# Optimization experiments

Measured on AMD Instinct MI355X. Metric: run time of the kernel, lower is better.

The kernel has to match this reference:

```python
import jax, jax.numpy as jnp
import numpy as np

EMBED_DIM = 384
NUM_HEADS = 6
EPS = 1e-5

def _conv_proj(x, w_dw, gamma, beta, mean, var, stride):
    # x: [B,H,W,C]; depthwise 3x3 conv (groups=C), pad 1, then BN (inference), then flatten HW.
    C = x.shape[-1]
    y = jax.lax.conv_general_dilated(
        x, w_dw, window_strides=(stride, stride), padding=[(1, 1), (1, 1)],
        dimension_numbers=("NHWC", "HWIO", "NHWC"), feature_group_count=C)
    y = (y - mean) * jax.lax.rsqrt(var + EPS) * gamma + beta
    B, H, W, Cc = y.shape
    return y.reshape(B, H * W, Cc)

def _heads(x):
    # [B, L, C] -> [B, nH, L, hd]
    B, L, C = x.shape
    hd = C // NUM_HEADS
    return x.reshape(B, L, NUM_HEADS, hd).transpose(0, 2, 1, 3)

def setup_inputs() -> dict:
    key = jax.random.key(0)
    ks = jax.random.split(key, 20)
    B, H, W, C = 64, 28, 28, EMBED_DIM
    inp = {
        "hidden_state": jax.random.normal(ks[0], (B, 1 + H * W, C), dtype=jnp.float32),
        "height": H,
        "width": W,
    }
    std = 0.02
    for i, p in enumerate(("q", "k", "v")):
        inp[f"w_dw_{p}"] = jax.random.normal(ks[1 + i], (3, 3, 1, C), dtype=jnp.float32) * std
        inp[f"bn_gamma_{p}"] = jnp.ones((C,), jnp.float32) + 0.1 * jax.random.normal(ks[4 + i], (C,))
        inp[f"bn_beta_{p}"] = 0.1 * jax.random.normal(ks[7 + i], (C,))
        inp[f"bn_mean_{p}"] = 0.1 * jax.random.normal(ks[10 + i], (C,))
        inp[f"bn_var_{p}"] = jnp.ones((C,), jnp.float32) + 0.1 * jax.random.uniform(ks[13 + i], (C,))
        inp[f"W_{p}"] = jax.random.normal(ks[16 + i], (C, C), dtype=jnp.float32) * std
        inp[f"b_{p}"] = jnp.zeros((C,), jnp.float32)
    return inp

def reference(hidden_state, height, width,
              w_dw_q, bn_gamma_q, bn_beta_q, bn_mean_q, bn_var_q, W_q, b_q,
              w_dw_k, bn_gamma_k, bn_beta_k, bn_mean_k, bn_var_k, W_k, b_k,
              w_dw_v, bn_gamma_v, bn_beta_v, bn_mean_v, bn_var_v, W_v, b_v):
    B, _, C = hidden_state.shape
    scale = C ** (-0.5)  # note: embed_dim**-0.5, as in the source
    cls_token = hidden_state[:, :1]
    x = hidden_state[:, 1:].reshape(B, height, width, C)

    q = _conv_proj(x, w_dw_q, bn_gamma_q, bn_beta_q, bn_mean_q, bn_var_q, stride=1)
    k = _conv_proj(x, w_dw_k, bn_gamma_k, bn_beta_k, bn_mean_k, bn_var_k, stride=2)
    v = _conv_proj(x, w_dw_v, bn_gamma_v, bn_beta_v, bn_mean_v, bn_var_v, stride=2)

    q = jnp.concatenate((cls_token, q), axis=1)
    k = jnp.concatenate((cls_token, k), axis=1)
    v = jnp.concatenate((cls_token, v), axis=1)

    q = _heads(q @ W_q + b_q)  # [B,h,Lq,d]
    k = _heads(k @ W_k + b_k)  # [B,h,Lk,d]
    v = _heads(v @ W_v + b_v)

    scores = jnp.einsum("bhqd,bhkd->bhqk", q, k) * scale
    probs = jax.nn.softmax(scores, axis=-1)
    ctx = jnp.einsum("bhqk,bhkd->bhqd", probs, v)
    Lq = ctx.shape[2]
    return ctx.transpose(0, 2, 1, 3).reshape(B, Lq, C)
```

## Files before the change

kernel.cpp:

```cpp
#include <hip/hip_runtime.h>
#include <hip/hip_bf16.h>

#define C_DIM 384
#define BATCH 64
#define LQ 785
#define LK 197
#define NHEADS 6
#define HDIM 64
#define QTILES 785
#define KTILES 197
#define KPAD 208

typedef __hip_bfloat16 bf16;
typedef __attribute__((ext_vector_type(8))) short short8;
typedef __attribute__((ext_vector_type(4))) float float4v;

__device__ __forceinline__ float bf2f(bf16 x) { return __bfloat162float(x); }
__device__ __forceinline__ bf16 f2bf(float x) { return __float2bfloat16(x); }
__device__ __forceinline__ float lo16f(unsigned int u) { return __uint_as_float(u << 16); }
__device__ __forceinline__ float hi16f(unsigned int u) { return __uint_as_float(u & 0xffff0000u); }
__device__ __forceinline__ unsigned short bfb(float x) {
    union { bf16 h; unsigned short s; } u; u.h = f2bf(x); return u.s;
}
__device__ __forceinline__ unsigned int pk2(float a, float b) {
    return ((unsigned int)bfb(b) << 16) | bfb(a);
}

template<bool F32>
__device__ __forceinline__ float ldx(const void* p, size_t i) {
    if constexpr (F32) return ((const float*)p)[i];
    else return bf2f(((const bf16*)p)[i]);
}
template<bool F32>
__device__ __forceinline__ void stx(void* p, size_t i, float v) {
    if constexpr (F32) ((float*)p)[i] = v;
    else ((bf16*)p)[i] = f2bf(v);
}
template<bool F32>
__device__ __forceinline__ void ld4(const void* p, size_t i, float* o) {
    if constexpr (F32) {
        float4 v = *(const float4*)((const float*)p + i);
        o[0] = v.x; o[1] = v.y; o[2] = v.z; o[3] = v.w;
    } else {
        uint2 u = *(const uint2*)((const bf16*)p + i);
        o[0] = lo16f(u.x); o[1] = hi16f(u.x); o[2] = lo16f(u.y); o[3] = hi16f(u.y);
    }
}
template<bool F32>
__device__ __forceinline__ void ld2(const void* p, size_t i, float* o) {
    if constexpr (F32) {
        float2 v = *(const float2*)((const float*)p + i);
        o[0] = v.x; o[1] = v.y;
    } else {
        unsigned int u = *(const unsigned int*)((const bf16*)p + i);
        o[0] = lo16f(u); o[1] = hi16f(u);
    }
}

__global__ void detect_kernel(const void* varq, int* flag) {
    const unsigned short* u = (const unsigned short*)varq;
    int votes = 0;
    #pragma unroll
    for (int i = 0; i < 4; ++i) {
        float b = __uint_as_float(((unsigned int)u[2 * i]) << 16);
        votes += (b > 0.5f && b < 2.0f) ? 1 : 0;
    }
    *flag = (votes == 4) ? 1 : 0;
}

template<bool F32>
__global__ __launch_bounds__(256) void repack_kernel(const int* __restrict__ flagp,
    const void* __restrict__ W0, const void* __restrict__ W1, const void* __restrict__ W2,
    bf16* __restrict__ dst)
{
    if (*flagp != (F32 ? 0 : 1)) return;
    const void* W = blockIdx.y == 0 ? W0 : (blockIdx.y == 1 ? W1 : W2);
    bf16* d = dst + (size_t)blockIdx.y * (C_DIM * C_DIM);
    int idx = blockIdx.x * 256 + threadIdx.x;
    int k = idx / C_DIM, nc = idx - k * C_DIM;
    int nt = nc >> 4, n = nc & 15, kt = k >> 5, q = (k >> 3) & 3, j = k & 7;
    d[(size_t)((((nt * 12 + kt) * 4 + q) * 16 + n) * 8 + j)] = f2bf(ldx<F32>(W, idx));
}

template<bool F32>
__device__ __forceinline__ void foldw(const void* __restrict__ wdw,
    const void* __restrict__ gamma, const void* __restrict__ beta,
    const void* __restrict__ mean,  const void* __restrict__ var,
    int c0, float w[9][2], float sh[2])
{
    float g[2], be[2], mu[2], vv[2];
    ld2<F32>(gamma, c0, g); ld2<F32>(beta, c0, be);
    ld2<F32>(mean,  c0, mu); ld2<F32>(var,  c0, vv);
    float sc[2];
    #pragma unroll
    for (int i = 0; i < 2; ++i) {
        sc[i] = g[i] * rsqrtf(vv[i] + 1e-5f);
        sh[i] = be[i] - mu[i] * sc[i];
    }
    #pragma unroll
    for (int p = 0; p < 9; ++p) {
        float t[2];
        ld2<F32>(wdw, (size_t)p * C_DIM + c0, t);
        w[p][0] = t[0] * sc[0];
        w[p][1] = t[1] * sc[1];
    }
}

template<int OJH, bool F32>
__device__ __forceinline__ void conv_quad(int b, int oik, int c2,
    const void* __restrict__ hs,
    const void* wq_, const void* gq, const void* beq, const void* muq, const void* vaq,
    const void* wk_, const void* gk, const void* bek, const void* muk, const void* vak,
    const void* wv_, const void* gv, const void* bev, const void* muv, const void* vav,
    bf16* __restrict__ qa, bf16* __restrict__ ka, bf16* __restrict__ va)
{
    int c0 = c2 * 2;
    float wq[9][2], wk[9][2], wv[9][2], shq[2], shk[2], shv[2];
    foldw<F32>(wq_, gq, beq, muq, vaq, c0, wq, shq);
    foldw<F32>(wk_, gk, bek, muk, vak, c0, wk, shk);
    foldw<F32>(wv_, gv, bev, muv, vav, c0, wv, shv);

    size_t hb = (size_t)b * (LQ * C_DIM);
    int i0 = 2 * oik - 1;
    bool rv[4];
    #pragma unroll
    for (int ri = 0; ri < 4; ++ri) rv[ri] = ((unsigned)(i0 + ri)) < 28u;

    float xw[4][3][2];
    constexpr int JJ0 = 14 * OJH - 1;

    int rq0 = b * LQ + 1 + 2 * oik * 28;
    int rq1 = rq0 + 28;
    int rk  = b * LK + 1 + oik * 14;

    #pragma unroll
    for (int s = 0; s < 16; ++s) {
        const int jj = JJ0 + s;
        const int sl = ((jj % 3) + 3) % 3;
        const bool cval = (jj >= 0) && (jj < 28);
        #pragma unroll
        for (int ri = 0; ri < 4; ++ri) {
            if (cval && rv[ri])
                ld2<F32>(hs, hb + (size_t)(1 + (i0 + ri) * 28 + jj) * C_DIM + c0, xw[ri][sl]);
            else { xw[ri][sl][0] = 0.f; xw[ri][sl][1] = 0.f; }
        }
        if (s >= 2) {
            const int jc = jj - 1;
            float a0[2] = {}, a1[2] = {};
            #pragma unroll
            for (int di = 0; di < 3; ++di)
                #pragma unroll
                for (int dj = 0; dj < 3; ++dj) {
                    const int s2 = (((jc - 1 + dj) % 3) + 3) % 3;
                    const int t = di * 3 + dj;
                    a0[0] = fmaf(xw[di][s2][0],     wq[t][0], a0[0]);
                    a0[1] = fmaf(xw[di][s2][1],     wq[t][1], a0[1]);
                    a1[0] = fmaf(xw[di + 1][s2][0], wq[t][0], a1[0]);
                    a1[1] = fmaf(xw[di + 1][s2][1], wq[t][1], a1[1]);
                }
            *(unsigned int*)&qa[(size_t)(rq0 + jc) * C_DIM + c0] = pk2(a0[0] + shq[0], a0[1] + shq[1]);
            *(unsigned int*)&qa[(size_t)(rq1 + jc) * C_DIM + c0] = pk2(a1[0] + shq[0], a1[1] + shq[1]);
            if ((jc & 1) == 0) {
                float k0[2] = {}, v0[2] = {};
                #pragma unroll
                for (int di = 0; di < 3; ++di)
                    #pragma unroll
                    for (int dj = 0; dj < 3; ++dj) {
                        const int s2 = (((jc - 1 + dj) % 3) + 3) % 3;
                        const int t = di * 3 + dj;
                        k0[0] = fmaf(xw[di][s2][0], wk[t][0], k0[0]);
                        k0[1] = fmaf(xw[di][s2][1], wk[t][1], k0[1]);
                        v0[0] = fmaf(xw[di][s2][0], wv[t][0], v0[0]);
                        v0[1] = fmaf(xw[di][s2][1], wv[t][1], v0[1]);
                    }
                int ro = rk + (jc >> 1);
                *(unsigned int*)&ka[(size_t)ro * C_DIM + c0] = pk2(k0[0] + shk[0], k0[1] + shk[1]);
                *(unsigned int*)&va[(size_t)ro * C_DIM + c0] = pk2(v0[0] + shv[0], v0[1] + shv[1]);
            }
        }
    }
}

#define CONV4_BLOCKS 960
template<bool F32>
__global__ __launch_bounds__(384) void conv4_kernel(
    const int* __restrict__ flagp, const void* __restrict__ hs,
    const void* wq, const void* gq, const void* beq, const void* muq, const void* vaq,
    const void* wk, const void* gk, const void* bek, const void* muk, const void* vak,
    const void* wv, const void* gv, const void* bev, const void* muv, const void* vav,
    bf16* __restrict__ qa, bf16* __restrict__ ka, bf16* __restrict__ va)
{
    if (*flagp != (F32 ? 0 : 1)) return;
    int bid = blockIdx.x;
    int tid = threadIdx.x;
    if (bid < 896) {
        int w = (bid & 7) * 112 + (bid >> 3);
        int b = w / 14, oik = w - b * 14;
        int c2 = tid % 192, ojh = tid / 192;
        if (ojh == 0)
            conv_quad<0, F32>(b, oik, c2, hs, wq, gq, beq, muq, vaq,
                              wk, gk, bek, muk, vak, wv, gv, bev, muv, vav, qa, ka, va);
        else
            conv_quad<1, F32>(b, oik, c2, hs, wq, gq, beq, muq, vaq,
                              wk, gk, bek, muk, vak, wv, gv, bev, muv, vav, qa, ka, va);
    } else {
        int b = bid - 896;
        if (tid < 192) {
            int c0 = tid * 2;
            float v2[2];
            ld2<F32>(hs, (size_t)b * (LQ * C_DIM) + c0, v2);
            unsigned int pk = pk2(v2[0], v2[1]);
            *(unsigned int*)&qa[(size_t)(b * LQ) * C_DIM + c0] = pk;
            *(unsigned int*)&ka[(size_t)(b * LK) * C_DIM + c0] = pk;
            *(unsigned int*)&va[(size_t)(b * LK) * C_DIM + c0] = pk;
        }
    }
}

__global__ __launch_bounds__(512) void gemm_lds_kernel(
    const int* __restrict__ flagp,
    bf16* __restrict__ qa, const bf16* __restrict__ ka, const bf16* __restrict__ va,
    const bf16* __restrict__ wrep,
    const void* __restrict__ b_q, const void* __restrict__ b_k, const void* __restrict__ b_v,
    bf16* __restrict__ kbuf, bf16* __restrict__ vbuf)
{
    __shared__ bf16 A_s[64 * C_DIM];

    const bool f32 = (*flagp == 0);
    int bidx = blockIdx.x;
    const bf16* A; const bf16* wr; const void* bias; int tile, mode;
    if (bidx < QTILES)                { mode = 0; tile = bidx;                  A = qa; wr = wrep;                          bias = b_q; }
    else if (bidx < QTILES + KTILES)  { mode = 1; tile = bidx - QTILES;         A = ka; wr = wrep + (size_t)C_DIM * C_DIM;     bias = b_k; }
    else                              { mode = 2; tile = bidx - QTILES - KTILES; A = va; wr = wrep + (size_t)2 * C_DIM * C_DIM; bias = b_v; }

    const bf16* Abase = A + (size_t)tile * (64 * C_DIM);
    int tid = threadIdx.x;
    int lane = tid & 63, wave = tid >> 6;
    int mrow = lane & 15, quad = lane >> 4;

    {
        int l4 = lane & 3, l16 = lane >> 2;
        #pragma unroll
        for (int i = 0; i < 6; ++i) {
            int t6 = wave * 6 + i;
            int rbase = (t6 / 3) * 4;
            int cbase = (t6 % 3) * 16;
            int row = rbase + l4;
            int ch  = cbase + l16;
            uint4 v = *(const uint4*)(Abase + (size_t)row * C_DIM + ch * 8);
            int dst = ch * 64 + (row ^ ((ch & 1) << 2));
            *(uint4*)&A_s[dst * 8] = v;
        }
    }
    __syncthreads();

    const short8* as = (const short8*)A_s;
    const short8* wf = (const short8*)wr;
    float4v acc[4][3] = {};

    #pragma unroll 2
    for (int kt = 0; kt < 12; ++kt) {
        short8 a[4];
        #pragma unroll
        for (int mt = 0; mt < 4; ++mt)
            a[mt] = as[(kt * 4 + quad) * 64 + ((mt * 16 + mrow) ^ ((quad & 1) << 2))];
        #pragma unroll
        for (int nt = 0; nt < 3; ++nt) {
            short8 bfrag = wf[(size_t)((wave * 3 + nt) * 12 + kt) * 64 + lane];
            #pragma unroll
            for (int mt = 0; mt < 4; ++mt)
                acc[mt][nt] = __builtin_amdgcn_mfma_f32_16x16x32_bf16(a[mt], bfrag, acc[mt][nt], 0, 0, 0);
        }
    }

    #pragma unroll
    for (int nt = 0; nt < 3; ++nt) {
        int col = wave * 48 + nt * 16 + mrow;
        float bb = f32 ? ((const float*)bias)[col] : bf2f(((const bf16*)bias)[col]);
        #pragma unroll
        for (int mt = 0; mt < 4; ++mt) {
            int row = tile * 64 + mt * 16 + quad * 4;
            #pragma unroll
            for (int r2 = 0; r2 < 4; ++r2) {
                float v = acc[mt][nt][r2] + bb;
                size_t o = (size_t)(row + r2) * C_DIM + col;
                if (mode == 0)      qa[o]   = f2bf(v);
                else if (mode == 1) kbuf[o] = f2bf(v);
                else                vbuf[o] = f2bf(v);
            }
        }
    }
}

__global__ __launch_bounds__(256) void vt_transpose_kernel(
    const bf16* __restrict__ v, bf16* __restrict__ vt)
{
    __shared__ unsigned short t[64][66];
    int bid = blockIdx.x;
    int ct = bid % 6; int tmp = bid / 6;
    int kt = tmp % 4; int b = tmp / 4;
    int k0 = kt * 64, c0 = ct * 64;
    int tid = threadIdx.x;

    for (int e = tid; e < 64 * 32; e += 256) {
        int r = e >> 5, c2 = e & 31;
        int k = k0 + r;
        unsigned int val = 0;
        if (k < LK) val = *(const unsigned int*)(v + ((size_t)b * LK + k) * C_DIM + c0 + c2 * 2);
        *(unsigned int*)&t[r][c2 * 2] = val;
    }
    __syncthreads();

    for (int e = tid; e < 64 * 32; e += 256) {
        int c = e >> 5, r2 = e & 31;
        int k = k0 + r2 * 2;
        if (k < KPAD) {
            unsigned int val = ((unsigned int)t[r2 * 2 + 1][c] << 16) | t[r2 * 2][c];
            *(unsigned int*)&vt[((size_t)(b * C_DIM + c0 + c)) * KPAD + k] = val;
        }
    }
}

template<int L, int OW, int STRIDE, bool F32, bool OF32>
__global__ __launch_bounds__(256) void fused_proj_kernel(
    const int* __restrict__ flagp,
    const void* __restrict__ hs, const void* __restrict__ wdw,
    const void* __restrict__ gamma, const void* __restrict__ beta,
    const void* __restrict__ mean,  const void* __restrict__ var,
    const bf16* __restrict__ Wrep,  const void* __restrict__ bias,
    void* __restrict__ O)
{
    if (*flagp != (F32 ? 0 : 1)) return;

    __shared__ bf16 A_s[64 * C_DIM];
    __shared__ float sc[C_DIM];
    __shared__ float sh[C_DIM];
    int tid = threadIdx.x;
    int m0 = blockIdx.x * 64;

    for (int c = tid; c < C_DIM; c += 256) {
        float s = ldx<F32>(gamma, c) * rsqrtf(ldx<F32>(var, c) + 1e-5f);
        sc[c] = s;
        sh[c] = ldx<F32>(beta, c) - ldx<F32>(mean, c) * s;
    }
    __syncthreads();

    for (int e = tid; e < 64 * 96; e += 256) {
        int m = e / 96;
        int c = (e - m * 96) * 4;
        int r = m0 + m;
        int b = r / L;
        int l = r - b * L;
        size_t hb = (size_t)b * (LQ * C_DIM);
        float v[4];
        if (l == 0) {
            ld4<F32>(hs, hb + c, v);
        } else {
            int p = l - 1;
            int oi = p / OW;
            int oj = p - oi * OW;
            float a0 = 0.f, a1 = 0.f, a2 = 0.f, a3 = 0.f;
            #pragma unroll
            for (int di = 0; di < 3; ++di) {
                int ii = oi * STRIDE - 1 + di;
                if (ii < 0 || ii >= 28) continue;
                #pragma unroll
                for (int dj = 0; dj < 3; ++dj) {
                    int jj = oj * STRIDE - 1 + dj;
                    if (jj < 0 || jj >= 28) continue;
                    float x[4], w[4];
                    ld4<F32>(hs, hb + (size_t)(1 + ii * 28 + jj) * C_DIM + c, x);
                    ld4<F32>(wdw, (size_t)(di * 3 + dj) * C_DIM + c, w);
                    a0 = fmaf(x[0], w[0], a0); a1 = fmaf(x[1], w[1], a1);
                    a2 = fmaf(x[2], w[2], a2); a3 = fmaf(x[3], w[3], a3);
                }
            }
            v[0] = a0 * sc[c + 0] + sh[c + 0];
            v[1] = a1 * sc[c + 1] + sh[c + 1];
            v[2] = a2 * sc[c + 2] + sh[c + 2];
            v[3] = a3 * sc[c + 3] + sh[c + 3];
        }
        int kt = c >> 5, q = (c >> 3) & 3, j = c & 7;
        int ofs = ((kt * 4 + q) * 64 + m) * 8 + j;
        ushort4 st = { bfb(v[0]), bfb(v[1]), bfb(v[2]), bfb(v[3]) };
        *(ushort4*)&A_s[ofs] = st;
    }
    __syncthreads();

    int lane = tid & 63, wave = tid >> 6;
    int mrow = lane & 15, quad = lane >> 4;
    float4v acc[4][6] = {};
    const short8* as = (const short8*)A_s;
    const short8* wr = (const short8*)Wrep;

    for (int kt = 0; kt < 12; ++kt) {
        short8 a[4];
        #pragma unroll
        for (int mt = 0; mt < 4; ++mt)
            a[mt] = as[(kt * 4 + quad) * 64 + mt * 16 + mrow];
        #pragma unroll
        for (int nt = 0; nt < 6; ++nt) {
            int ntg = wave * 6 + nt;
            short8 bfrag = wr[(size_t)(ntg * 12 + kt) * 64 + lane];
            #pragma unroll
            for (int mt = 0; mt < 4; ++mt)
                acc[mt][nt] = __builtin_amdgcn_mfma_f32_16x16x32_bf16(a[mt], bfrag, acc[mt][nt], 0, 0, 0);
        }
    }

    #pragma unroll
    for (int nt = 0; nt < 6; ++nt) {
        int col = wave * 96 + nt * 16 + mrow;
        float bb = ldx<F32>(bias, col);
        #pragma unroll
        for (int mt = 0; mt < 4; ++mt) {
            int row = m0 + mt * 16 + quad * 4;
            #pragma unroll
            for (int r2 = 0; r2 < 4; ++r2)
                stx<OF32>(O, (size_t)(row + r2) * C_DIM + col, acc[mt][nt][r2] + bb);
        }
    }
}

__global__ __launch_bounds__(256) void attn_vt2_kernel(
    const int* __restrict__ flagp,
    const bf16* __restrict__ qg,
    const bf16* __restrict__ kg,
    const bf16* __restrict__ vt_g,
    void* __restrict__ out)
{
    __shared__ unsigned short Kf[8 * 2 * 64 * 8];
    __shared__ unsigned short Vt[64 * 128];
    __shared__ unsigned short Ps[4 * 16 * 128];

    const bool f32 = (*flagp == 0);
    int tid = threadIdx.x;
    int lane = tid & 63, wave = tid >> 6;
    int m = lane & 15, quad = lane >> 4;
    int bid = blockIdx.x;
    int w = (bid & 7) * 624 + (bid >> 3);
    int qb = w % 13;
    int bh = w / 13;
    int h = bh % NHEADS, b = bh / NHEADS;
    int qbase = qb * 64 + wave * 16;

    int qrow = min(qbase + m, LQ - 1);
    const bf16* qp = qg + ((size_t)b * LQ + qrow) * C_DIM + h * HDIM;
    short8 bq[2];
    bq[0] = *(const short8*)(qp + quad * 8);
    bq[1] = *(const short8*)(qp + 32 + quad * 8);

    const float scale = 0.05103103630798287f;
    float4v ctx[4] = {};
    float lsum = 0.f;
    size_t kvbase = (size_t)b * LK * C_DIM + h * HDIM;
    size_t vtbase = (size_t)(b * C_DIM + h * HDIM) * KPAD;

    for (int c = 0; c < 2; ++c) {
        int c0 = c * 128;
        for (int e = tid; e < 1024; e += 256) {
            int col = e >> 3, d8 = e & 7;
            int gcol = c0 + col;
            uint4 val = {0, 0, 0, 0};
            if (gcol < LK) val = *(const uint4*)(kg + kvbase + (size_t)gcol * C_DIM + d8 * 8);
            int nt = col >> 4, n = col & 15, ks = d8 >> 2, q = d8 & 3;
            *(uint4*)&Kf[((nt * 2 + ks) * 64 + q * 16 + n) * 8] = val;
        }
        for (int e = tid; e < 1024; e += 256) {
            int d = e >> 4, kc = e & 15;
            uint4 val = {0, 0, 0, 0};
            if (c0 + kc * 8 < KPAD)
                val = *(const uint4*)(vt_g + vtbase + (size_t)d * KPAD + c0 + kc * 8);
            *(uint4*)&Vt[(d << 7) + ((kc ^ (d & 15)) << 3)] = val;
        }
        __syncthreads();

        const short8* kf = (const short8*)Kf;
        unsigned short* pw = Ps + wave * (16 * 128);
        int ntmax = (c == 0) ? 8 : 5;
        for (int nt = 0; nt < ntmax; ++nt) {
            float4v s = {0.f, 0.f, 0.f, 0.f};
            s = __builtin_amdgcn_mfma_f32_16x16x32_bf16(kf[(nt * 2 + 0) * 64 + lane], bq[0], s, 0, 0, 0);
            s = __builtin_amdgcn_mfma_f32_16x16x32_bf16(kf[(nt * 2 + 1) * 64 + lane], bq[1], s, 0, 0, 0);
            int kb = c0 + nt * 16 + quad * 4;
            float pv[4];
            #pragma unroll
            for (int r = 0; r < 4; ++r) {
                pv[r] = (kb + r < LK) ? __expf(s[r] * scale) : 0.f;
                lsum += pv[r];
            }
            int chunk = (nt * 2 + (quad >> 1)) ^ m;
            uint2 pk; pk.x = pk2(pv[0], pv[1]); pk.y = pk2(pv[2], pv[3]);
            *(uint2*)&pw[m * 128 + chunk * 8 + (quad & 1) * 4] = pk;
        }
        if (c == 1) {
            uint2 z = {0, 0};
            #pragma unroll
            for (int nt = 5; nt < 8; ++nt) {
                int chunk = (nt * 2 + (quad >> 1)) ^ m;
                *(uint2*)&pw[m * 128 + chunk * 8 + (quad & 1) * 4] = z;
            }
        }

        const short8* vts = (const short8*)Vt;
        const short8* pf = (const short8*)Ps;
        #pragma unroll
        for (int ks = 0; ks < 4; ++ks) {
            short8 ap = pf[wave * 256 + m * 16 + ((ks * 4 + quad) ^ m)];
            #pragma unroll
            for (int ntv = 0; ntv < 4; ++ntv) {
                short8 bf_ = vts[((ntv * 16 + m) << 4) + ((ks * 4 + quad) ^ m)];
                ctx[ntv] = __builtin_amdgcn_mfma_f32_16x16x32_bf16(ap, bf_, ctx[ntv], 0, 0, 0);
            }
        }
        __syncthreads();
    }

    lsum += __shfl_xor(lsum, 16);
    lsum += __shfl_xor(lsum, 32);
    float inv = 1.f / lsum;

    #pragma unroll
    for (int ntv = 0; ntv < 4; ++ntv) {
        #pragma unroll
        for (int r = 0; r < 4; ++r) {
            int row = qbase + quad * 4 + r;
            float iv = __shfl(inv, quad * 4 + r);
            if (row < LQ) {
                size_t o = ((size_t)b * LQ + row) * C_DIM + h * HDIM + ntv * 16 + m;
                float v = ctx[ntv][r] * iv;
                if (f32) ((float*)out)[o] = v;
                else     ((bf16*)out)[o] = f2bf(v);
            }
        }
    }
}

template<bool F32>
__global__ __launch_bounds__(256) void attn_kernel(
    const int* __restrict__ flagp,
    const bf16* __restrict__ kg,
    const bf16* __restrict__ vg,
    void* __restrict__ qo)
{
    if (*flagp != (F32 ? 0 : 1)) return;

    __shared__ unsigned short Kf[8 * 2 * 64 * 8];
    __shared__ unsigned short Vf[4 * 4 * 64 * 8];
    __shared__ unsigned short Ps[4 * 16 * 136];

    int tid = threadIdx.x;
    int lane = tid & 63, wave = tid >> 6;
    int m = lane & 15, quad = lane >> 4;
    int bid = blockIdx.x;
    int qb = bid % 13;
    int bh = bid / 13;
    int h = bh % NHEADS, b = bh / NHEADS;
    int qbase = qb * 64 + wave * 16;

    int qrow = min(qbase + m, LQ - 1);
    size_t qoff = ((size_t)b * LQ + qrow) * C_DIM + h * HDIM;
    short8 aq[2];
    #pragma unroll
    for (int ks = 0; ks < 2; ++ks) {
        float t[8];
        ld4<F32>(qo, qoff + ks * 32 + quad * 8, t);
        ld4<F32>(qo, qoff + ks * 32 + quad * 8 + 4, t + 4);
        short8 f;
        #pragma unroll
        for (int j = 0; j < 8; ++j) f[j] = (short)bfb(t[j]);
        aq[ks] = f;
    }

    const float scale = 0.05103103630798287f;
    float4v ctx[4] = {};
    float lsum4[4] = {};
    size_t kvbase = (size_t)b * LK * C_DIM + h * HDIM;

    for (int c = 0; c < 2; ++c) {
        int c0 = c * 128;
        for (int e = tid; e < 1024; e += 256) {
            int col = e >> 3, d8 = e & 7;
            int gcol = c0 + col;
            uint4 val = {0, 0, 0, 0};
            if (gcol < LK) val = *(const uint4*)(kg + kvbase + (size_t)gcol * C_DIM + d8 * 8);
            int nt = col >> 4, n = col & 15, ks = d8 >> 2, q = d8 & 3;
            *(uint4*)&Kf[((nt * 2 + ks) * 64 + q * 16 + n) * 8] = val;
        }
        for (int e = tid; e < 1024; e += 256) {
            int p = e >> 3, d8 = e & 7;
            int gp = c0 + p;
            int ks = p >> 5, q = (p >> 3) & 3, j = p & 7;
            int ntv = d8 >> 1, nl0 = (d8 & 1) * 8;
            if (gp < LK) {
                union { uint4 u; unsigned short s[8]; } val;
                val.u = *(const uint4*)(vg + kvbase + (size_t)gp * C_DIM + d8 * 8);
                #pragma unroll
                for (int i = 0; i < 8; ++i)
                    Vf[((ntv * 4 + ks) * 64 + q * 16 + nl0 + i) * 8 + j] = val.s[i];
            } else {
                #pragma unroll
                for (int i = 0; i < 8; ++i)
                    Vf[((ntv * 4 + ks) * 64 + q * 16 + nl0 + i) * 8 + j] = 0;
            }
        }
        __syncthreads();

        const short8* kf = (const short8*)Kf;
        unsigned short* pw = Ps + wave * (16 * 136);
        int ntmax = (c == 0) ? 8 : 5;
        for (int nt = 0; nt < ntmax; ++nt) {
            float4v s = {0.f, 0.f, 0.f, 0.f};
            #pragma unroll
            for (int ks = 0; ks < 2; ++ks)
                s = __builtin_amdgcn_mfma_f32_16x16x32_bf16(aq[ks], kf[(nt * 2 + ks) * 64 + lane], s, 0, 0, 0);
            int coln = c0 + nt * 16 + m;
            bool valid = coln < LK;
            #pragma unroll
            for (int r = 0; r < 4; ++r) {
                float pv = valid ? __expf(s[r] * scale) : 0.f;
                lsum4[r] += pv;
                pw[(quad * 4 + r) * 136 + nt * 16 + m] = bfb(pv);
            }
        }
        if (c == 1) {
            #pragma unroll
            for (int nt = 5; nt < 8; ++nt)
                #pragma unroll
                for (int r = 0; r < 4; ++r)
                    pw[(quad * 4 + r) * 136 + nt * 16 + m] = 0;
        }

        const short8* vf = (const short8*)Vf;
        const short8* pf = (const short8*)Ps;
        #pragma unroll
        for (int ks = 0; ks < 4; ++ks) {
            short8 ap = pf[wave * 272 + m * 17 + ks * 4 + quad];
            #pragma unroll
            for (int ntv = 0; ntv < 4; ++ntv)
                ctx[ntv] = __builtin_amdgcn_mfma_f32_16x16x32_bf16(ap, vf[(ntv * 4 + ks) * 64 + lane], ctx[ntv], 0, 0, 0);
        }
        __syncthreads();
    }

    float inv[4];
    #pragma unroll
    for (int r = 0; r < 4; ++r) {
        float t = lsum4[r];
        t += __shfl_xor(t, 1);
        t += __shfl_xor(t, 2);
        t += __shfl_xor(t, 4);
        t += __shfl_xor(t, 8);
        inv[r] = 1.f / t;
    }
    #pragma unroll
    for (int ntv = 0; ntv < 4; ++ntv) {
        #pragma unroll
        for (int r = 0; r < 4; ++r) {
            int row = qbase + quad * 4 + r;
            if (row < LQ)
                stx<F32>(qo, ((size_t)b * LQ + row) * C_DIM + h * HDIM + ntv * 16 + m, ctx[ntv][r] * inv[r]);
        }
    }
}

extern "C" void kernel_launch(void* const* d_in, const int* in_sizes, int n_in,
                              void* d_out, int out_size, void* d_ws, size_t ws_size,
                              hipStream_t stream)
{
    const void* hs    = d_in[0];
    const void* wdw_q = d_in[3];
    const void* g_q   = d_in[4];
    const void* be_q  = d_in[5];
    const void* mu_q  = d_in[6];
    const void* va_q  = d_in[7];
    const void* W_q   = d_in[8];
    const void* b_q   = d_in[9];
    const void* wdw_k = d_in[10];
    const void* g_k   = d_in[11];
    const void* be_k  = d_in[12];
    const void* mu_k  = d_in[13];
    const void* va_k  = d_in[14];
    const void* W_k   = d_in[15];
    const void* b_k   = d_in[16];
    const void* wdw_v = d_in[17];
    const void* g_v   = d_in[18];
    const void* be_v  = d_in[19];
    const void* mu_v  = d_in[20];
    const void* va_v  = d_in[21];
    const void* W_v   = d_in[22];
    const void* b_v   = d_in[23];

    const size_t QA = (size_t)QTILES * 24576;
    const size_t KA = (size_t)KTILES * 24576;
    const size_t NEED_BIG = 16 + 2 * (3 * (size_t)C_DIM * C_DIM + QA + 4 * KA);

    int*  flag = (int*)d_ws;
    bf16* wrep = (bf16*)((char*)d_ws + 16);
    bf16* wrq  = wrep;
    bf16* wrk  = wrep + (size_t)C_DIM * C_DIM;
    bf16* wrv  = wrep + (size_t)2 * C_DIM * C_DIM;

    detect_kernel<<<1, 1, 0, stream>>>(va_q, flag);
    repack_kernel<false><<<dim3(576, 3), 256, 0, stream>>>(flag, W_q, W_k, W_v, wrep);
    repack_kernel<true ><<<dim3(576, 3), 256, 0, stream>>>(flag, W_q, W_k, W_v, wrep);

    if (ws_size >= NEED_BIG) {
        bf16* qa    = wrep + (size_t)3 * C_DIM * C_DIM;
        bf16* ka    = qa + QA;
        bf16* vaa   = ka + KA;
        bf16* kbuf  = vaa + KA;
        bf16* vbuf  = kbuf + KA;
        bf16* vbuft = ka;

        conv4_kernel<false><<<CONV4_BLOCKS, 384, 0, stream>>>(flag, hs,
            wdw_q, g_q, be_q, mu_q, va_q, wdw_k, g_k, be_k, mu_k, va_k,
            wdw_v, g_v, be_v, mu_v, va_v, qa, ka, vaa);
        conv4_kernel<true ><<<CONV4_BLOCKS, 384, 0, stream>>>(flag, hs,
            wdw_q, g_q, be_q, mu_q, va_q, wdw_k, g_k, be_k, mu_k, va_k,
            wdw_v, g_v, be_v, mu_v, va_v, qa, ka, vaa);

        gemm_lds_kernel<<<QTILES + 2 * KTILES, 512, 0, stream>>>(flag,
            qa, ka, vaa, wrep, b_q, b_k, b_v, kbuf, vbuf);

        vt_transpose_kernel<<<BATCH * 24, 256, 0, stream>>>(vbuf, vbuft);

        attn_vt2_kernel<<<384 * 13, 256, 0, stream>>>(flag, qa, kbuf, vbuft, d_out);
    } else {
        bf16* kbuf = wrep + (size_t)3 * C_DIM * C_DIM;
        bf16* vbuf = kbuf + (size_t)BATCH * LK * C_DIM;

        fused_proj_kernel<LQ, 28, 1, false, false><<<LQ, 256, 0, stream>>>(flag, hs, wdw_q, g_q, be_q, mu_q, va_q, wrq, b_q, d_out);
        fused_proj_kernel<LQ, 28, 1, true,  true ><<<LQ, 256, 0, stream>>>(flag, hs, wdw_q, g_q, be_q, mu_q, va_q, wrq, b_q, d_out);
        fused_proj_kernel<LK, 14, 2, false, false><<<LK, 256, 0, stream>>>(flag, hs, wdw_k, g_k, be_k, mu_k, va_k, wrk, b_k, kbuf);
        fused_proj_kernel<LK, 14, 2, true,  false><<<LK, 256, 0, stream>>>(flag, hs, wdw_k, g_k, be_k, mu_k, va_k, wrk, b_k, kbuf);
        fused_proj_kernel<LK, 14, 2, false, false><<<LK, 256, 0, stream>>>(flag, hs, wdw_v, g_v, be_v, mu_v, va_v, wrv, b_v, vbuf);
        fused_proj_kernel<LK, 14, 2, true,  false><<<LK, 256, 0, stream>>>(flag, hs, wdw_v, g_v, be_v, mu_v, va_v, wrv, b_v, vbuf);

        attn_kernel<false><<<384 * 13, 256, 0, stream>>>(flag, kbuf, vbuf, d_out);
        attn_kernel<true ><<<384 * 13, 256, 0, stream>>>(flag, kbuf, vbuf, d_out);
    }
}
```

Before: 333.5 us.

## Read K/V directly from global in attention, merge dtype-dispatched launches

The attention kernel no longer stages K and transposed V tiles through shared memory in two chunks with barriers. Each wave now loads K fragments and V^T fragments straight from global (L2-cached) memory, and keeps only the probability tile in LDS. The V transpose padding grows to 224 so all 7 k-steps can be read without bounds checks. The repack and conv kernels are each merged into one launch that branches on the runtime dtype flag, which removes the duplicate no-op launches at the cost of larger kernel code.

```diff
diff --git a/kernel.cpp b/kernel.cpp
--- a/kernel.cpp
+++ b/kernel.cpp
@@ -9,7 +9,7 @@
 #define HDIM 64
 #define QTILES 785
 #define KTILES 197
-#define KPAD 208
+#define KPAD 224
 
 typedef __hip_bfloat16 bf16;
 typedef __attribute__((ext_vector_type(8))) short short8;
@@ -68,18 +68,18 @@
     *flag = (votes == 4) ? 1 : 0;
 }
 
-template<bool F32>
 __global__ __launch_bounds__(256) void repack_kernel(const int* __restrict__ flagp,
     const void* __restrict__ W0, const void* __restrict__ W1, const void* __restrict__ W2,
     bf16* __restrict__ dst)
 {
-    if (*flagp != (F32 ? 0 : 1)) return;
+    const bool f32 = (*flagp == 0);
     const void* W = blockIdx.y == 0 ? W0 : (blockIdx.y == 1 ? W1 : W2);
     bf16* d = dst + (size_t)blockIdx.y * (C_DIM * C_DIM);
     int idx = blockIdx.x * 256 + threadIdx.x;
     int k = idx / C_DIM, nc = idx - k * C_DIM;
     int nt = nc >> 4, n = nc & 15, kt = k >> 5, q = (k >> 3) & 3, j = k & 7;
-    d[(size_t)((((nt * 12 + kt) * 4 + q) * 16 + n) * 8 + j)] = f2bf(ldx<F32>(W, idx));
+    float v = f32 ? ((const float*)W)[idx] : bf2f(((const bf16*)W)[idx]);
+    d[(size_t)((((nt * 12 + kt) * 4 + q) * 16 + n) * 8 + j)] = f2bf(v);
 }
 
 template<bool F32>
@@ -182,7 +182,6 @@
 }
 
 #define CONV4_BLOCKS 960
-template<bool F32>
 __global__ __launch_bounds__(384) void conv4_kernel(
     const int* __restrict__ flagp, const void* __restrict__ hs,
     const void* wq, const void* gq, const void* beq, const void* muq, const void* vaq,
@@ -190,25 +189,35 @@
     const void* wv, const void* gv, const void* bev, const void* muv, const void* vav,
     bf16* __restrict__ qa, bf16* __restrict__ ka, bf16* __restrict__ va)
 {
-    if (*flagp != (F32 ? 0 : 1)) return;
+    const bool f32 = (*flagp == 0);
     int bid = blockIdx.x;
     int tid = threadIdx.x;
     if (bid < 896) {
         int w = (bid & 7) * 112 + (bid >> 3);
         int b = w / 14, oik = w - b * 14;
         int c2 = tid % 192, ojh = tid / 192;
-        if (ojh == 0)
-            conv_quad<0, F32>(b, oik, c2, hs, wq, gq, beq, muq, vaq,
-                              wk, gk, bek, muk, vak, wv, gv, bev, muv, vav, qa, ka, va);
-        else
-            conv_quad<1, F32>(b, oik, c2, hs, wq, gq, beq, muq, vaq,
-                              wk, gk, bek, muk, vak, wv, gv, bev, muv, vav, qa, ka, va);
+        if (f32) {
+            if (ojh == 0)
+                conv_quad<0, true>(b, oik, c2, hs, wq, gq, beq, muq, vaq,
+                                   wk, gk, bek, muk, vak, wv, gv, bev, muv, vav, qa, ka, va);
+            else
+                conv_quad<1, true>(b, oik, c2, hs, wq, gq, beq, muq, vaq,
+                                   wk, gk, bek, muk, vak, wv, gv, bev, muv, vav, qa, ka, va);
+        } else {
+            if (ojh == 0)
+                conv_quad<0, false>(b, oik, c2, hs, wq, gq, beq, muq, vaq,
+                                    wk, gk, bek, muk, vak, wv, gv, bev, muv, vav, qa, ka, va);
+            else
+                conv_quad<1, false>(b, oik, c2, hs, wq, gq, beq, muq, vaq,
+                                    wk, gk, bek, muk, vak, wv, gv, bev, muv, vav, qa, ka, va);
+        }
     } else {
         int b = bid - 896;
         if (tid < 192) {
             int c0 = tid * 2;
             float v2[2];
-            ld2<F32>(hs, (size_t)b * (LQ * C_DIM) + c0, v2);
+            if (f32) ld2<true>(hs, (size_t)b * (LQ * C_DIM) + c0, v2);
+            else     ld2<false>(hs, (size_t)b * (LQ * C_DIM) + c0, v2);
             unsigned int pk = pk2(v2[0], v2[1]);
             *(unsigned int*)&qa[(size_t)(b * LQ) * C_DIM + c0] = pk;
             *(unsigned int*)&ka[(size_t)(b * LK) * C_DIM + c0] = pk;
@@ -422,16 +431,14 @@
     }
 }
 
-__global__ __launch_bounds__(256) void attn_vt2_kernel(
+__global__ __launch_bounds__(256) void attn_vt3_kernel(
     const int* __restrict__ flagp,
     const bf16* __restrict__ qg,
     const bf16* __restrict__ kg,
     const bf16* __restrict__ vt_g,
     void* __restrict__ out)
 {
-    __shared__ unsigned short Kf[8 * 2 * 64 * 8];
-    __shared__ unsigned short Vt[64 * 128];
-    __shared__ unsigned short Ps[4 * 16 * 128];
+    __shared__ unsigned short Ps[4 * 16 * 32 * 8];
 
     const bool f32 = (*flagp == 0);
     int tid = threadIdx.x;
@@ -451,69 +458,47 @@
     bq[1] = *(const short8*)(qp + 32 + quad * 8);
 
     const float scale = 0.05103103630798287f;
-    float4v ctx[4] = {};
-    float lsum = 0.f;
     size_t kvbase = (size_t)b * LK * C_DIM + h * HDIM;
     size_t vtbase = (size_t)(b * C_DIM + h * HDIM) * KPAD;
 
-    for (int c = 0; c < 2; ++c) {
-        int c0 = c * 128;
-        for (int e = tid; e < 1024; e += 256) {
-            int col = e >> 3, d8 = e & 7;
-            int gcol = c0 + col;
-            uint4 val = {0, 0, 0, 0};
-            if (gcol < LK) val = *(const uint4*)(kg + kvbase + (size_t)gcol * C_DIM + d8 * 8);
-            int nt = col >> 4, n = col & 15, ks = d8 >> 2, q = d8 & 3;
-            *(uint4*)&Kf[((nt * 2 + ks) * 64 + q * 16 + n) * 8] = val;
-        }
-        for (int e = tid; e < 1024; e += 256) {
-            int d = e >> 4, kc = e & 15;
-            uint4 val = {0, 0, 0, 0};
-            if (c0 + kc * 8 < KPAD)
-                val = *(const uint4*)(vt_g + vtbase + (size_t)d * KPAD + c0 + kc * 8);
-            *(uint4*)&Vt[(d << 7) + ((kc ^ (d & 15)) << 3)] = val;
-        }
-        __syncthreads();
-
-        const short8* kf = (const short8*)Kf;
-        unsigned short* pw = Ps + wave * (16 * 128);
-        int ntmax = (c == 0) ? 8 : 5;
-        for (int nt = 0; nt < ntmax; ++nt) {
-            float4v s = {0.f, 0.f, 0.f, 0.f};
-            s = __builtin_amdgcn_mfma_f32_16x16x32_bf16(kf[(nt * 2 + 0) * 64 + lane], bq[0], s, 0, 0, 0);
-            s = __builtin_amdgcn_mfma_f32_16x16x32_bf16(kf[(nt * 2 + 1) * 64 + lane], bq[1], s, 0, 0, 0);
-            int kb = c0 + nt * 16 + quad * 4;
-            float pv[4];
-            #pragma unroll
-            for (int r = 0; r < 4; ++r) {
-                pv[r] = (kb + r < LK) ? __expf(s[r] * scale) : 0.f;
-                lsum += pv[r];
-            }
-            int chunk = (nt * 2 + (quad >> 1)) ^ m;
-            uint2 pk; pk.x = pk2(pv[0], pv[1]); pk.y = pk2(pv[2], pv[3]);
-            *(uint2*)&pw[m * 128 + chunk * 8 + (quad & 1) * 4] = pk;
-        }
-        if (c == 1) {
-            uint2 z = {0, 0};
-            #pragma unroll
-            for (int nt = 5; nt < 8; ++nt) {
-                int chunk = (nt * 2 + (quad >> 1)) ^ m;
-                *(uint2*)&pw[m * 128 + chunk * 8 + (quad & 1) * 4] = z;
-            }
-        }
-
-        const short8* vts = (const short8*)Vt;
-        const short8* pf = (const short8*)Ps;
-        #pragma unroll
-        for (int ks = 0; ks < 4; ++ks) {
-            short8 ap = pf[wave * 256 + m * 16 + ((ks * 4 + quad) ^ m)];
-            #pragma unroll
-            for (int ntv = 0; ntv < 4; ++ntv) {
-                short8 bf_ = vts[((ntv * 16 + m) << 4) + ((ks * 4 + quad) ^ m)];
-                ctx[ntv] = __builtin_amdgcn_mfma_f32_16x16x32_bf16(ap, bf_, ctx[ntv], 0, 0, 0);
-            }
-        }
-        __syncthreads();
+    unsigned short* pw = Ps + wave * 4096;
+    float lsum = 0.f;
+
+    #pragma unroll 2
+    for (int nt = 0; nt < 13; ++nt) {
+        int krow = min(nt * 16 + m, LK - 1);
+        const bf16* kp = kg + kvbase + (size_t)krow * C_DIM;
+        float4v s = {0.f, 0.f, 0.f, 0.f};
+        s = __builtin_amdgcn_mfma_f32_16x16x32_bf16(*(const short8*)(kp + quad * 8),      bq[0], s, 0, 0, 0);
+        s = __builtin_amdgcn_mfma_f32_16x16x32_bf16(*(const short8*)(kp + 32 + quad * 8), bq[1], s, 0, 0, 0);
+        int kb = nt * 16 + quad * 4;
+        float pv[4];
+        #pragma unroll
+        for (int r = 0; r < 4; ++r) {
+            pv[r] = (kb + r < LK) ? __expf(s[r] * scale) : 0.f;
+            lsum += pv[r];
+        }
+        int chunk = (nt * 2 + (quad >> 1)) ^ m;
+        uint2 pk; pk.x = pk2(pv[0], pv[1]); pk.y = pk2(pv[2], pv[3]);
+        *(uint2*)&pw[m * 256 + chunk * 8 + (quad & 1) * 4] = pk;
+    }
+    {
+        uint2 z = {0, 0};
+        int chunk = (26 + (quad >> 1)) ^ m;
+        *(uint2*)&pw[m * 256 + chunk * 8 + (quad & 1) * 4] = z;
+    }
+
+    float4v ctx[4] = {};
+    const short8* pf = (const short8*)Ps;
+    const bf16* vp = vt_g + vtbase;
+    #pragma unroll 2
+    for (int ks = 0; ks < 7; ++ks) {
+        short8 ap = pf[wave * 512 + m * 32 + ((ks * 4 + quad) ^ m)];
+        #pragma unroll
+        for (int ntv = 0; ntv < 4; ++ntv) {
+            short8 bf_ = *(const short8*)(vp + (size_t)(ntv * 16 + m) * KPAD + ks * 32 + quad * 8);
+            ctx[ntv] = __builtin_amdgcn_mfma_f32_16x16x32_bf16(ap, bf_, ctx[ntv], 0, 0, 0);
+        }
     }
 
     lsum += __shfl_xor(lsum, 16);
@@ -702,8 +687,7 @@
     bf16* wrv  = wrep + (size_t)2 * C_DIM * C_DIM;
 
     detect_kernel<<<1, 1, 0, stream>>>(va_q, flag);
-    repack_kernel<false><<<dim3(576, 3), 256, 0, stream>>>(flag, W_q, W_k, W_v, wrep);
-    repack_kernel<true ><<<dim3(576, 3), 256, 0, stream>>>(flag, W_q, W_k, W_v, wrep);
+    repack_kernel<<<dim3(576, 3), 256, 0, stream>>>(flag, W_q, W_k, W_v, wrep);
 
     if (ws_size >= NEED_BIG) {
         bf16* qa    = wrep + (size_t)3 * C_DIM * C_DIM;
@@ -713,19 +697,16 @@
         bf16* vbuf  = kbuf + KA;
         bf16* vbuft = ka;
 
-        conv4_kernel<false><<<CONV4_BLOCKS, 384, 0, stream>>>(flag, hs,
+        conv4_kernel<<<CONV4_BLOCKS, 384, 0, stream>>>(flag, hs,
             wdw_q, g_q, be_q, mu_q, va_q, wdw_k, g_k, be_k, mu_k, va_k,
             wdw_v, g_v, be_v, mu_v, va_v, qa, ka, vaa);
-        conv4_kernel<true ><<<CONV4_BLOCKS, 384, 0, stream>>>(flag, hs,
-            wdw_q, g_q, be_q, mu_q, va_q, wdw_k, g_k, be_k, mu_k, va_k,
-            wdw_v, g_v, be_v, mu_v, va_v, qa, ka, vaa);
 
         gemm_lds_kernel<<<QTILES + 2 * KTILES, 512, 0, stream>>>(flag,
             qa, ka, vaa, wrep, b_q, b_k, b_v, kbuf, vbuf);
 
         vt_transpose_kernel<<<BATCH * 24, 256, 0, stream>>>(vbuf, vbuft);
 
-        attn_vt2_kernel<<<384 * 13, 256, 0, stream>>>(flag, qa, kbuf, vbuft, d_out);
+        attn_vt3_kernel<<<384 * 13, 256, 0, stream>>>(flag, qa, kbuf, vbuft, d_out);
     } else {
         bf16* kbuf = wrep + (size_t)3 * C_DIM * C_DIM;
         bf16* vbuf = kbuf + (size_t)BATCH * LK * C_DIM;
```

Result: slower. 362.3 us (+8.6%).

## Merge dtype-specialized launches and widen attention blocks to 128 query rows

Applied to the files above, without the earlier changes.

The repack and conv kernels no longer come in two templated launches that early-exit on a dtype flag. Each is now a single launch that branches on the flag inside the kernel. The attention kernel moves from 256 to 512 threads, with 8 waves covering 128 query rows per block. This halves how many times each K/V chunk is staged into shared memory per (batch, head) and cuts the launch count. The trade-offs are more LDS per block (a larger Ps buffer), possibly lower occupancy, more wasted padded rows in the last query tile, and code bloat from the runtime dtype branch.

```diff
diff --git a/kernel.cpp b/kernel.cpp
--- a/kernel.cpp
+++ b/kernel.cpp
@@ -68,18 +68,18 @@
     *flag = (votes == 4) ? 1 : 0;
 }
 
-template<bool F32>
 __global__ __launch_bounds__(256) void repack_kernel(const int* __restrict__ flagp,
     const void* __restrict__ W0, const void* __restrict__ W1, const void* __restrict__ W2,
     bf16* __restrict__ dst)
 {
-    if (*flagp != (F32 ? 0 : 1)) return;
+    const bool f32 = (*flagp == 0);
     const void* W = blockIdx.y == 0 ? W0 : (blockIdx.y == 1 ? W1 : W2);
     bf16* d = dst + (size_t)blockIdx.y * (C_DIM * C_DIM);
     int idx = blockIdx.x * 256 + threadIdx.x;
     int k = idx / C_DIM, nc = idx - k * C_DIM;
     int nt = nc >> 4, n = nc & 15, kt = k >> 5, q = (k >> 3) & 3, j = k & 7;
-    d[(size_t)((((nt * 12 + kt) * 4 + q) * 16 + n) * 8 + j)] = f2bf(ldx<F32>(W, idx));
+    float v = f32 ? ((const float*)W)[idx] : bf2f(((const bf16*)W)[idx]);
+    d[(size_t)((((nt * 12 + kt) * 4 + q) * 16 + n) * 8 + j)] = f2bf(v);
 }
 
 template<bool F32>
@@ -182,7 +182,6 @@
 }
 
 #define CONV4_BLOCKS 960
-template<bool F32>
 __global__ __launch_bounds__(384) void conv4_kernel(
     const int* __restrict__ flagp, const void* __restrict__ hs,
     const void* wq, const void* gq, const void* beq, const void* muq, const void* vaq,
@@ -190,25 +189,35 @@
     const void* wv, const void* gv, const void* bev, const void* muv, const void* vav,
     bf16* __restrict__ qa, bf16* __restrict__ ka, bf16* __restrict__ va)
 {
-    if (*flagp != (F32 ? 0 : 1)) return;
+    const bool f32 = (*flagp == 0);
     int bid = blockIdx.x;
     int tid = threadIdx.x;
     if (bid < 896) {
         int w = (bid & 7) * 112 + (bid >> 3);
         int b = w / 14, oik = w - b * 14;
         int c2 = tid % 192, ojh = tid / 192;
-        if (ojh == 0)
-            conv_quad<0, F32>(b, oik, c2, hs, wq, gq, beq, muq, vaq,
-                              wk, gk, bek, muk, vak, wv, gv, bev, muv, vav, qa, ka, va);
-        else
-            conv_quad<1, F32>(b, oik, c2, hs, wq, gq, beq, muq, vaq,
-                              wk, gk, bek, muk, vak, wv, gv, bev, muv, vav, qa, ka, va);
+        if (f32) {
+            if (ojh == 0)
+                conv_quad<0, true>(b, oik, c2, hs, wq, gq, beq, muq, vaq,
+                                   wk, gk, bek, muk, vak, wv, gv, bev, muv, vav, qa, ka, va);
+            else
+                conv_quad<1, true>(b, oik, c2, hs, wq, gq, beq, muq, vaq,
+                                   wk, gk, bek, muk, vak, wv, gv, bev, muv, vav, qa, ka, va);
+        } else {
+            if (ojh == 0)
+                conv_quad<0, false>(b, oik, c2, hs, wq, gq, beq, muq, vaq,
+                                    wk, gk, bek, muk, vak, wv, gv, bev, muv, vav, qa, ka, va);
+            else
+                conv_quad<1, false>(b, oik, c2, hs, wq, gq, beq, muq, vaq,
+                                    wk, gk, bek, muk, vak, wv, gv, bev, muv, vav, qa, ka, va);
+        }
     } else {
         int b = bid - 896;
         if (tid < 192) {
             int c0 = tid * 2;
             float v2[2];
-            ld2<F32>(hs, (size_t)b * (LQ * C_DIM) + c0, v2);
+            if (f32) ld2<true>(hs, (size_t)b * (LQ * C_DIM) + c0, v2);
+            else     ld2<false>(hs, (size_t)b * (LQ * C_DIM) + c0, v2);
             unsigned int pk = pk2(v2[0], v2[1]);
             *(unsigned int*)&qa[(size_t)(b * LQ) * C_DIM + c0] = pk;
             *(unsigned int*)&ka[(size_t)(b * LK) * C_DIM + c0] = pk;
@@ -422,7 +431,7 @@
     }
 }
 
-__global__ __launch_bounds__(256) void attn_vt2_kernel(
+__global__ __launch_bounds__(512) void attn_vt4_kernel(
     const int* __restrict__ flagp,
     const bf16* __restrict__ qg,
     const bf16* __restrict__ kg,
@@ -431,18 +440,18 @@
 {
     __shared__ unsigned short Kf[8 * 2 * 64 * 8];
     __shared__ unsigned short Vt[64 * 128];
-    __shared__ unsigned short Ps[4 * 16 * 128];
+    __shared__ unsigned short Ps[8 * 16 * 128];
 
     const bool f32 = (*flagp == 0);
     int tid = threadIdx.x;
     int lane = tid & 63, wave = tid >> 6;
     int m = lane & 15, quad = lane >> 4;
     int bid = blockIdx.x;
-    int w = (bid & 7) * 624 + (bid >> 3);
-    int qb = w % 13;
-    int bh = w / 13;
+    int w = (bid & 7) * 336 + (bid >> 3);
+    int qsb = w % 7;
+    int bh = w / 7;
     int h = bh % NHEADS, b = bh / NHEADS;
-    int qbase = qb * 64 + wave * 16;
+    int qbase = qsb * 128 + wave * 16;
 
     int qrow = min(qbase + m, LQ - 1);
     const bf16* qp = qg + ((size_t)b * LQ + qrow) * C_DIM + h * HDIM;
@@ -458,7 +467,7 @@
 
     for (int c = 0; c < 2; ++c) {
         int c0 = c * 128;
-        for (int e = tid; e < 1024; e += 256) {
+        for (int e = tid; e < 1024; e += 512) {
             int col = e >> 3, d8 = e & 7;
             int gcol = c0 + col;
             uint4 val = {0, 0, 0, 0};
@@ -466,7 +475,7 @@
             int nt = col >> 4, n = col & 15, ks = d8 >> 2, q = d8 & 3;
             *(uint4*)&Kf[((nt * 2 + ks) * 64 + q * 16 + n) * 8] = val;
         }
-        for (int e = tid; e < 1024; e += 256) {
+        for (int e = tid; e < 1024; e += 512) {
             int d = e >> 4, kc = e & 15;
             uint4 val = {0, 0, 0, 0};
             if (c0 + kc * 8 < KPAD)
@@ -702,8 +711,7 @@
     bf16* wrv  = wrep + (size_t)2 * C_DIM * C_DIM;
 
     detect_kernel<<<1, 1, 0, stream>>>(va_q, flag);
-    repack_kernel<false><<<dim3(576, 3), 256, 0, stream>>>(flag, W_q, W_k, W_v, wrep);
-    repack_kernel<true ><<<dim3(576, 3), 256, 0, stream>>>(flag, W_q, W_k, W_v, wrep);
+    repack_kernel<<<dim3(576, 3), 256, 0, stream>>>(flag, W_q, W_k, W_v, wrep);
 
     if (ws_size >= NEED_BIG) {
         bf16* qa    = wrep + (size_t)3 * C_DIM * C_DIM;
@@ -713,19 +721,16 @@
         bf16* vbuf  = kbuf + KA;
         bf16* vbuft = ka;
 
-        conv4_kernel<false><<<CONV4_BLOCKS, 384, 0, stream>>>(flag, hs,
+        conv4_kernel<<<CONV4_BLOCKS, 384, 0, stream>>>(flag, hs,
             wdw_q, g_q, be_q, mu_q, va_q, wdw_k, g_k, be_k, mu_k, va_k,
             wdw_v, g_v, be_v, mu_v, va_v, qa, ka, vaa);
-        conv4_kernel<true ><<<CONV4_BLOCKS, 384, 0, stream>>>(flag, hs,
-            wdw_q, g_q, be_q, mu_q, va_q, wdw_k, g_k, be_k, mu_k, va_k,
-            wdw_v, g_v, be_v, mu_v, va_v, qa, ka, vaa);
 
         gemm_lds_kernel<<<QTILES + 2 * KTILES, 512, 0, stream>>>(flag,
             qa, ka, vaa, wrep, b_q, b_k, b_v, kbuf, vbuf);
 
         vt_transpose_kernel<<<BATCH * 24, 256, 0, stream>>>(vbuf, vbuft);
 
-        attn_vt2_kernel<<<384 * 13, 256, 0, stream>>>(flag, qa, kbuf, vbuft, d_out);
+        attn_vt4_kernel<<<384 * 7, 512, 0, stream>>>(flag, qa, kbuf, vbuft, d_out);
     } else {
         bf16* kbuf = wrep + (size_t)3 * C_DIM * C_DIM;
         bf16* vbuf = kbuf + (size_t)BATCH * LK * C_DIM;
```

Measured after the change: 318.2 us. 4.6% less time.
